# Performance work log

Hardware: AMD Instinct MI355X
Metric: run time of the kernel (lower is better)

## Reference

```python
import jax, jax.numpy as jnp
import numpy as np

EPS = 1e-5

def _ln(x, g, b):
    m = jnp.mean(x, axis=-1, keepdims=True)
    v = jnp.var(x, axis=-1, keepdims=True)
    return (x - m) / jnp.sqrt(v + EPS) * g + b

def setup_inputs() -> dict:
    key = jax.random.key(0)
    ks = jax.random.split(key, 16)
    B, N, CZ, C = 1, 512, 128, 16
    s_cz = 1.0 / np.sqrt(CZ)
    s_c = 1.0 / np.sqrt(C)
    def lin(k, fan_in, shape):
        return jax.random.uniform(k, shape, jnp.float32, -1.0, 1.0) / np.sqrt(fan_in)
    return {
        'x': jax.random.normal(ks[0], (B, N, N, CZ), jnp.float32),
        'Wa1': lin(ks[1], CZ, (CZ, C)), 'ba1': lin(ks[2], CZ, (C,)),
        'Wa2': lin(ks[3], CZ, (CZ, C)), 'ba2': lin(ks[4], CZ, (C,)),
        'Wb1': lin(ks[5], CZ, (CZ, C)), 'bb1': lin(ks[6], CZ, (C,)),
        'Wb2': lin(ks[7], CZ, (CZ, C)), 'bb2': lin(ks[8], CZ, (C,)),
        'ln2_g': jnp.ones((C,), jnp.float32), 'ln2_b': jnp.zeros((C,), jnp.float32),
        'Wg': lin(ks[9], CZ, (CZ, CZ)), 'bg': lin(ks[10], CZ, (CZ,)),
        'Wz': lin(ks[11], C, (C, CZ)), 'bz': lin(ks[12], C, (CZ,)),
    }

def reference(x, Wa1, ba1, Wa2, ba2, Wb1, bb1, Wb2, bb2, ln2_g, ln2_b, Wg, bg, Wz, bz):
    # NOTE: original code computes z=ln1(x) then overwrites z=x, so ln1 is a no-op.
    direction = 'outgoing'
    a = jax.nn.sigmoid((x @ Wa1 + ba1) * (x @ Wa2 + ba2))  # [B,N,N,c]
    b = jax.nn.sigmoid((x @ Wb1 + bb1) * (x @ Wb2 + bb2))  # [B,N,N,c]
    if direction == 'incoming':
        a = jnp.swapaxes(a, 1, 2)
        b = jnp.swapaxes(b, 1, 2)
    g = jax.nn.sigmoid(x @ Wg + bg)  # [B,N,N,c_z]
    # z[b,i,j,c] = sum_k a[b,i,k,c] * b[b,k,j,c]  (per-channel triangle matmul)
    z = jnp.einsum('bikc,bkjc->bijc', a, b)
    return g * (_ln(z, ln2_g, ln2_b) @ Wz + bz)
```

## Files before the change

### kernel.cpp

```cpp
#include <hip/hip_runtime.h>


#define NN 512
#define PP (NN*NN)
#define CZD 128
#define CD 16
#define LN_EPS 1e-5f

typedef unsigned short u16;
typedef __bf16 bf16x8 __attribute__((ext_vector_type(8)));
typedef float  f32x4  __attribute__((ext_vector_type(4)));

#define OFF_A  0u
#define OFF_B  8388608u
#define OFF_Z  16777216u
#define OFF_G  33554432u
#define OFF_WT 100663296u
#define OFF_BC 100712448u

__device__ __forceinline__ float bf2f(u16 u) {
    union { unsigned int i; float f; } v; v.i = ((unsigned int)u) << 16; return v.f;
}
__device__ __forceinline__ u16 f2bf(float f) {
    union { float f; unsigned int i; } v; v.f = f;
    unsigned int r = (v.i + 0x7FFFu + ((v.i >> 16) & 1u)) >> 16;
    return (u16)r;
}
__device__ __forceinline__ float sigmoidf(float x) { return 1.0f / (1.0f + __expf(-x)); }

__global__ void pack_w(const float* __restrict__ Wa1, const float* __restrict__ Wa2,
                       const float* __restrict__ Wb1, const float* __restrict__ Wb2,
                       const float* __restrict__ Wg,
                       const float* __restrict__ ba1, const float* __restrict__ ba2,
                       const float* __restrict__ bb1, const float* __restrict__ bb2,
                       const float* __restrict__ bg,
                       u16* __restrict__ wt, float* __restrict__ bc) {
    int idx = blockIdx.x * 256 + threadIdx.x;
    int n = idx >> 7, k = idx & 127;
    float v;
    if      (n < 16) v = Wa1[k * CD + n];
    else if (n < 32) v = Wa2[k * CD + (n - 16)];
    else if (n < 48) v = Wb1[k * CD + (n - 32)];
    else if (n < 64) v = Wb2[k * CD + (n - 48)];
    else             v = Wg [k * CZD + (n - 64)];
    wt[n * CZD + k] = f2bf(v);
    if (idx < 192) {
        float b;
        if      (idx < 16) b = ba1[idx];
        else if (idx < 32) b = ba2[idx - 16];
        else if (idx < 48) b = bb1[idx - 32];
        else if (idx < 64) b = bb2[idx - 48];
        else               b = bg [idx - 64];
        bc[idx] = b;
    }
}

__global__ __launch_bounds__(256) void proj_kernel(const float* __restrict__ x,
                                                   const u16* __restrict__ wt,
                                                   const float* __restrict__ bc,
                                                   u16* __restrict__ a_ws, u16* __restrict__ b_ws,
                                                   u16* __restrict__ g_ws) {
    __shared__ __align__(16) u16 Xlds[32][136];
    const int t = threadIdx.x;
    const int wave = t >> 6, lane = t & 63;
    const int l16 = lane & 15, quad = lane >> 4;
    const int rt = wave & 1, cg = wave >> 1;
    const long rowBase = (long)blockIdx.x * 32;

#pragma unroll
    for (int i = 0; i < 2; ++i) {
        int chunk = t + 256 * i;
        int r = chunk >> 4, ko = (chunk & 15) << 3;
        const float* xp = x + (rowBase + r) * CZD + ko;
        const float4 v0 = *reinterpret_cast<const float4*>(xp);
        const float4 v1 = *reinterpret_cast<const float4*>(xp + 4);
        u16 tmp[8] = { f2bf(v0.x), f2bf(v0.y), f2bf(v0.z), f2bf(v0.w),
                       f2bf(v1.x), f2bf(v1.y), f2bf(v1.z), f2bf(v1.w) };
        *reinterpret_cast<uint4*>(&Xlds[r][ko]) = *reinterpret_cast<const uint4*>(tmp);
    }
    bf16x8 wb[6][4];
#pragma unroll
    for (int ct = 0; ct < 6; ++ct) {
        int n = cg * 96 + ct * 16 + l16;
#pragma unroll
        for (int ks = 0; ks < 4; ++ks)
            wb[ct][ks] = *reinterpret_cast<const bf16x8*>(wt + n * CZD + ks * 32 + quad * 8);
    }
    __syncthreads();

    f32x4 acc[6];
#pragma unroll
    for (int ct = 0; ct < 6; ++ct) acc[ct] = (f32x4){0.f, 0.f, 0.f, 0.f};
#pragma unroll
    for (int ks = 0; ks < 4; ++ks) {
        bf16x8 af = *reinterpret_cast<const bf16x8*>(&Xlds[rt * 16 + l16][ks * 32 + quad * 8]);
#pragma unroll
        for (int ct = 0; ct < 6; ++ct)
            acc[ct] = __builtin_amdgcn_mfma_f32_16x16x32_bf16(af, wb[ct][ks], acc[ct], 0, 0, 0);
    }

    const int rl = rt * 16 + quad * 4;
    if (cg == 0) {
        const float b0 = bc[l16], b1 = bc[16 + l16], b2 = bc[32 + l16], b3 = bc[48 + l16];
        const float b4 = bc[64 + l16], b5 = bc[80 + l16];
#pragma unroll
        for (int r = 0; r < 4; ++r) {
            long pos = rowBase + rl + r;
            float av = sigmoidf((acc[0][r] + b0) * (acc[1][r] + b1));
            float bv = sigmoidf((acc[2][r] + b2) * (acc[3][r] + b3));
            a_ws[(long)l16 * PP + pos] = f2bf(av);
            b_ws[(long)l16 * PP + pos] = f2bf(bv);
            g_ws[pos * CZD + l16]      = f2bf(sigmoidf(acc[4][r] + b4));
            g_ws[pos * CZD + 16 + l16] = f2bf(sigmoidf(acc[5][r] + b5));
        }
    } else {
        float bb[6];
#pragma unroll
        for (int ct = 0; ct < 6; ++ct) bb[ct] = bc[96 + ct * 16 + l16];
#pragma unroll
        for (int r = 0; r < 4; ++r) {
            long pos = rowBase + rl + r;
#pragma unroll
            for (int ct = 0; ct < 6; ++ct)
                g_ws[pos * CZD + 32 + ct * 16 + l16] = f2bf(sigmoidf(acc[ct][r] + bb[ct]));
        }
    }
}

__global__ __launch_bounds__(256) void tri_kernel(const u16* __restrict__ a_ws,
                                                  const u16* __restrict__ b_ws,
                                                  float* __restrict__ z_ws) {
    __shared__ __align__(16) u16 Alds[64][72];
    __shared__ __align__(16) u16 Btl[64][72];
    const int t = threadIdx.x;
    const int wave = t >> 6, lane = t & 63, l16 = lane & 15, quad = lane >> 4;
    const int c = blockIdx.y;
    const int i0 = (blockIdx.x >> 3) * 64, j0 = (blockIdx.x & 7) * 64;
    const u16* Ap = a_ws + (long)c * PP;
    const u16* Bp = b_ws + (long)c * PP;

    f32x4 acc[4];
#pragma unroll
    for (int ct = 0; ct < 4; ++ct) acc[ct] = (f32x4){0.f, 0.f, 0.f, 0.f};

    for (int k0 = 0; k0 < NN; k0 += 64) {
#pragma unroll
        for (int i = 0; i < 2; ++i) {
            int chunk = t + 256 * i;
            int r = chunk >> 3, ko = (chunk & 7) << 3;
            uint4 v = *reinterpret_cast<const uint4*>(Ap + (long)(i0 + r) * NN + k0 + ko);
            *reinterpret_cast<uint4*>(&Alds[r][ko]) = v;
        }
#pragma unroll
        for (int i = 0; i < 2; ++i) {
            int chunk = t + 256 * i;
            int j = chunk & 63, kg = chunk >> 6;
            u16 tmp[8];
#pragma unroll
            for (int kk = 0; kk < 8; ++kk)
                tmp[kk] = Bp[(long)(k0 + kg * 8 + kk) * NN + j0 + j];
            *reinterpret_cast<uint4*>(&Btl[j][(kg ^ (j & 7)) << 3]) = *reinterpret_cast<uint4*>(tmp);
        }
        __syncthreads();
#pragma unroll
        for (int kk = 0; kk < 64; kk += 32) {
            bf16x8 af = *reinterpret_cast<const bf16x8*>(&Alds[wave * 16 + l16][kk + quad * 8]);
            int kc = (kk >> 3) + quad;
#pragma unroll
            for (int ct = 0; ct < 4; ++ct) {
                int n = ct * 16 + l16;
                bf16x8 bfv = *reinterpret_cast<const bf16x8*>(&Btl[n][(kc ^ (n & 7)) << 3]);
                acc[ct] = __builtin_amdgcn_mfma_f32_16x16x32_bf16(af, bfv, acc[ct], 0, 0, 0);
            }
        }
        __syncthreads();
    }
    float* Zp = z_ws + (long)c * PP;
#pragma unroll
    for (int ct = 0; ct < 4; ++ct)
#pragma unroll
        for (int r = 0; r < 4; ++r)
            Zp[(long)(i0 + wave * 16 + quad * 4 + r) * NN + j0 + ct * 16 + l16] = acc[ct][r];
}

__global__ __launch_bounds__(256) void out_kernel(const float* __restrict__ z_ws,
                                                  const u16* __restrict__ g_ws,
                                                  const float* __restrict__ Wz, const float* __restrict__ bz,
                                                  const float* __restrict__ lng, const float* __restrict__ lnb,
                                                  float* __restrict__ out) {
    __shared__ __align__(16) float zt[16][72];
    __shared__ __align__(16) float nl[64][20];
    __shared__ __align__(16) float wz[16][128];
    __shared__ float bzl[128];
    __shared__ float lg[16], lb[16];
    const int t = threadIdx.x;
    const long pos0 = (long)blockIdx.x * 64;

    {
        int cc = t >> 4, off = (t & 15) << 2;
        const float4 v = *reinterpret_cast<const float4*>(z_ws + (long)cc * PP + pos0 + off);
        *reinterpret_cast<float4*>(&zt[cc][off]) = v;
    }
#pragma unroll
    for (int i = 0; i < 8; ++i) {
        int idx = t + 256 * i;
        wz[idx >> 7][idx & 127] = Wz[idx];
    }
    if (t < 128)      bzl[t] = bz[t];
    else if (t < 144) lg[t - 128] = lng[t - 128];
    else if (t < 160) lb[t - 144] = lnb[t - 144];
    __syncthreads();

    {
        int p = t & 63, cgr = t >> 6;
        float m = 0.f;
#pragma unroll
        for (int c0 = 0; c0 < 16; ++c0) m += zt[c0][p];
        m *= (1.f / 16.f);
        float v = 0.f;
#pragma unroll
        for (int c0 = 0; c0 < 16; ++c0) { float d = zt[c0][p] - m; v += d * d; }
        v *= (1.f / 16.f);
        float s = rsqrtf(v + LN_EPS);
#pragma unroll
        for (int cc = 0; cc < 4; ++cc) {
            int c0 = cgr * 4 + cc;
            nl[p][c0] = (zt[c0][p] - m) * s * lg[c0] + lb[c0];
        }
    }
    __syncthreads();

    const int cz = t & 127, pg = t >> 7;
    float wzr[16];
#pragma unroll
    for (int c0 = 0; c0 < 16; ++c0) wzr[c0] = wz[c0][cz];
    const float bzv = bzl[cz];
#pragma unroll
    for (int pp2 = 0; pp2 < 32; ++pp2) {
        int p = pg * 32 + pp2;
        const float4* np = reinterpret_cast<const float4*>(&nl[p][0]);
        float y = bzv;
#pragma unroll
        for (int c4 = 0; c4 < 4; ++c4) {
            float4 nv = np[c4];
            y += nv.x * wzr[c4 * 4 + 0] + nv.y * wzr[c4 * 4 + 1] +
                 nv.z * wzr[c4 * 4 + 2] + nv.w * wzr[c4 * 4 + 3];
        }
        long o = (pos0 + p) * CZD + cz;
        float gv = bf2f(g_ws[o]);
        out[o] = gv * y;
    }
}

extern "C" void kernel_launch(void* const* d_in, const int* in_sizes, int n_in,
                              void* d_out, int out_size, void* d_ws, size_t ws_size,
                              hipStream_t stream) {
    const float* x   = (const float*)d_in[0];
    const float* Wa1 = (const float*)d_in[1];
    const float* ba1 = (const float*)d_in[2];
    const float* Wa2 = (const float*)d_in[3];
    const float* ba2 = (const float*)d_in[4];
    const float* Wb1 = (const float*)d_in[5];
    const float* bb1 = (const float*)d_in[6];
    const float* Wb2 = (const float*)d_in[7];
    const float* bb2 = (const float*)d_in[8];
    const float* lng = (const float*)d_in[9];
    const float* lnb = (const float*)d_in[10];
    const float* Wg  = (const float*)d_in[11];
    const float* bg  = (const float*)d_in[12];
    const float* Wz  = (const float*)d_in[13];
    const float* bz  = (const float*)d_in[14];
    float* out = (float*)d_out;
    char* ws = (char*)d_ws;
    u16*   a_ws = (u16*)(ws + OFF_A);
    u16*   b_ws = (u16*)(ws + OFF_B);
    float* z_ws = (float*)(ws + OFF_Z);
    u16*   g_ws = (u16*)(ws + OFF_G);
    u16*   wt   = (u16*)(ws + OFF_WT);
    float* bc   = (float*)(ws + OFF_BC);

    hipLaunchKernelGGL(pack_w, dim3(96), dim3(256), 0, stream,
                       Wa1, Wa2, Wb1, Wb2, Wg, ba1, ba2, bb1, bb2, bg, wt, bc);
    hipLaunchKernelGGL(proj_kernel, dim3(8192), dim3(256), 0, stream, x, wt, bc, a_ws, b_ws, g_ws);
    hipLaunchKernelGGL(tri_kernel, dim3(64, 16), dim3(256), 0, stream, a_ws, b_ws, z_ws);
    hipLaunchKernelGGL(out_kernel, dim3(4096), dim3(256), 0, stream, z_ws, g_ws, Wz, bz, lng, lnb, out);
}
```

Measured before the change: 372.3 us.

## Transpose B once, enlarge triangle-matmul tiles, and coalesce projection stores via LDS

The projection kernel now processes 64 rows per block with all 192 output columns per wave. It stages the a, b and g results in shared memory so they go to global memory as coalesced 16-byte stores instead of scattered 2-byte writes. A new transpose kernel writes b in k-contiguous layout, reusing the z workspace as scratch. The triangle matmul uses 128x128 tiles with a 4x4 MFMA grid per wave and register prefetch of the next k-tile, which replaces strided scalar gathers of b and improves data reuse. The cost is an extra kernel launch with a read and write pass over b, plus higher register and LDS use that may lower occupancy.

```diff
diff --git a/kernel.cpp b/kernel.cpp
--- a/kernel.cpp
+++ b/kernel.cpp
@@ -11,12 +11,12 @@
 typedef __bf16 bf16x8 __attribute__((ext_vector_type(8)));
 typedef float  f32x4  __attribute__((ext_vector_type(4)));
 
-#define OFF_A  0u
-#define OFF_B  8388608u
-#define OFF_Z  16777216u
-#define OFF_G  33554432u
-#define OFF_WT 100663296u
-#define OFF_BC 100712448u
+#define OFF_A   0u
+#define OFF_BT  8388608u
+#define OFF_Z   16777216u
+#define OFF_G   33554432u
+#define OFF_WT  100663296u
+#define OFF_BC  100712448u
 
 __device__ __forceinline__ float bf2f(u16 u) {
     union { unsigned int i; float f; } v; v.i = ((unsigned int)u) << 16; return v.f;
@@ -60,127 +60,177 @@
                                                    const float* __restrict__ bc,
                                                    u16* __restrict__ a_ws, u16* __restrict__ b_ws,
                                                    u16* __restrict__ g_ws) {
-    __shared__ __align__(16) u16 Xlds[32][136];
+    __shared__ __align__(16) u16 Xl[64][136];
+    __shared__ __align__(16) u16 at[16][72];
+    __shared__ __align__(16) u16 btl[16][72];
+    __shared__ __align__(16) u16 gt[64][136];
     const int t = threadIdx.x;
-    const int wave = t >> 6, lane = t & 63;
-    const int l16 = lane & 15, quad = lane >> 4;
-    const int rt = wave & 1, cg = wave >> 1;
-    const long rowBase = (long)blockIdx.x * 32;
-
-#pragma unroll
-    for (int i = 0; i < 2; ++i) {
-        int chunk = t + 256 * i;
-        int r = chunk >> 4, ko = (chunk & 15) << 3;
-        const float* xp = x + (rowBase + r) * CZD + ko;
+    const int rt = t >> 6, lane = t & 63, l16 = lane & 15, quad = lane >> 4;
+    const long R0 = (long)blockIdx.x * 64;
+
+#pragma unroll
+    for (int i = 0; i < 4; ++i) {
+        int ch = t + 256 * i;
+        int r = ch >> 4, ko = (ch & 15) << 3;
+        const float* xp = x + (R0 + r) * CZD + ko;
         const float4 v0 = *reinterpret_cast<const float4*>(xp);
         const float4 v1 = *reinterpret_cast<const float4*>(xp + 4);
         u16 tmp[8] = { f2bf(v0.x), f2bf(v0.y), f2bf(v0.z), f2bf(v0.w),
                        f2bf(v1.x), f2bf(v1.y), f2bf(v1.z), f2bf(v1.w) };
-        *reinterpret_cast<uint4*>(&Xlds[r][ko]) = *reinterpret_cast<const uint4*>(tmp);
-    }
-    bf16x8 wb[6][4];
-#pragma unroll
-    for (int ct = 0; ct < 6; ++ct) {
-        int n = cg * 96 + ct * 16 + l16;
-#pragma unroll
-        for (int ks = 0; ks < 4; ++ks)
-            wb[ct][ks] = *reinterpret_cast<const bf16x8*>(wt + n * CZD + ks * 32 + quad * 8);
-    }
-    __syncthreads();
-
-    f32x4 acc[6];
-#pragma unroll
-    for (int ct = 0; ct < 6; ++ct) acc[ct] = (f32x4){0.f, 0.f, 0.f, 0.f};
+        *reinterpret_cast<uint4*>(&Xl[r][ko]) = *reinterpret_cast<const uint4*>(tmp);
+    }
+    const float bA1 = bc[l16], bA2 = bc[16 + l16], bB1 = bc[32 + l16], bB2 = bc[48 + l16];
+    float bG[8];
+#pragma unroll
+    for (int c2 = 0; c2 < 8; ++c2) bG[c2] = bc[64 + c2 * 16 + l16];
+    __syncthreads();
+
+    f32x4 acc[12];
+#pragma unroll
+    for (int ct = 0; ct < 12; ++ct) acc[ct] = (f32x4){0.f, 0.f, 0.f, 0.f};
 #pragma unroll
     for (int ks = 0; ks < 4; ++ks) {
-        bf16x8 af = *reinterpret_cast<const bf16x8*>(&Xlds[rt * 16 + l16][ks * 32 + quad * 8]);
-#pragma unroll
-        for (int ct = 0; ct < 6; ++ct)
-            acc[ct] = __builtin_amdgcn_mfma_f32_16x16x32_bf16(af, wb[ct][ks], acc[ct], 0, 0, 0);
-    }
-
-    const int rl = rt * 16 + quad * 4;
-    if (cg == 0) {
-        const float b0 = bc[l16], b1 = bc[16 + l16], b2 = bc[32 + l16], b3 = bc[48 + l16];
-        const float b4 = bc[64 + l16], b5 = bc[80 + l16];
-#pragma unroll
-        for (int r = 0; r < 4; ++r) {
-            long pos = rowBase + rl + r;
-            float av = sigmoidf((acc[0][r] + b0) * (acc[1][r] + b1));
-            float bv = sigmoidf((acc[2][r] + b2) * (acc[3][r] + b3));
-            a_ws[(long)l16 * PP + pos] = f2bf(av);
-            b_ws[(long)l16 * PP + pos] = f2bf(bv);
-            g_ws[pos * CZD + l16]      = f2bf(sigmoidf(acc[4][r] + b4));
-            g_ws[pos * CZD + 16 + l16] = f2bf(sigmoidf(acc[5][r] + b5));
-        }
+        bf16x8 af = *reinterpret_cast<const bf16x8*>(&Xl[rt * 16 + l16][ks * 32 + quad * 8]);
+#pragma unroll
+        for (int ct = 0; ct < 12; ++ct) {
+            bf16x8 wf = *reinterpret_cast<const bf16x8*>(wt + (ct * 16 + l16) * CZD + ks * 32 + quad * 8);
+            acc[ct] = __builtin_amdgcn_mfma_f32_16x16x32_bf16(af, wf, acc[ct], 0, 0, 0);
+        }
+    }
+
+#pragma unroll
+    for (int r = 0; r < 4; ++r) {
+        int row = rt * 16 + quad * 4 + r;
+        float av = sigmoidf((acc[0][r] + bA1) * (acc[1][r] + bA2));
+        float bv = sigmoidf((acc[2][r] + bB1) * (acc[3][r] + bB2));
+        at[l16][row]  = f2bf(av);
+        btl[l16][row] = f2bf(bv);
+#pragma unroll
+        for (int c2 = 0; c2 < 8; ++c2)
+            gt[row][c2 * 16 + l16] = f2bf(sigmoidf(acc[4 + c2][r] + bG[c2]));
+    }
+    __syncthreads();
+
+    if (t < 128) {
+        int c = t >> 3, ch = t & 7;
+        *reinterpret_cast<uint4*>(a_ws + (long)c * PP + R0 + ch * 8) =
+            *reinterpret_cast<const uint4*>(&at[c][ch * 8]);
     } else {
-        float bb[6];
-#pragma unroll
-        for (int ct = 0; ct < 6; ++ct) bb[ct] = bc[96 + ct * 16 + l16];
-#pragma unroll
-        for (int r = 0; r < 4; ++r) {
-            long pos = rowBase + rl + r;
-#pragma unroll
-            for (int ct = 0; ct < 6; ++ct)
-                g_ws[pos * CZD + 32 + ct * 16 + l16] = f2bf(sigmoidf(acc[ct][r] + bb[ct]));
-        }
+        int c = (t - 128) >> 3, ch = (t - 128) & 7;
+        *reinterpret_cast<uint4*>(b_ws + (long)c * PP + R0 + ch * 8) =
+            *reinterpret_cast<const uint4*>(&btl[c][ch * 8]);
+    }
+#pragma unroll
+    for (int i = 0; i < 4; ++i) {
+        int ch = t + 256 * i;
+        int row = ch >> 4, co = (ch & 15) << 3;
+        *reinterpret_cast<uint4*>(g_ws + (R0 + row) * CZD + co) =
+            *reinterpret_cast<const uint4*>(&gt[row][co]);
+    }
+}
+
+__global__ __launch_bounds__(256) void transpose_b(const u16* __restrict__ b_ws,
+                                                   u16* __restrict__ bt_ws) {
+    __shared__ __align__(16) u16 T[64][72];
+    const int t = threadIdx.x;
+    const int c = blockIdx.y;
+    const int ty = blockIdx.x >> 3, tx = blockIdx.x & 7;
+    const int r0 = ty * 64, c0 = tx * 64;
+    const u16* Bp = b_ws + (long)c * PP;
+    u16* Tp = bt_ws + (long)c * PP;
+#pragma unroll
+    for (int i = 0; i < 2; ++i) {
+        int ch = t + 256 * i;
+        int r = ch >> 3, cc = ch & 7;
+        uint4 v = *reinterpret_cast<const uint4*>(Bp + (long)(r0 + r) * NN + c0 + cc * 8);
+        *reinterpret_cast<uint4*>(&T[r][(cc ^ (r >> 3)) << 3]) = v;
+    }
+    __syncthreads();
+#pragma unroll
+    for (int i = 0; i < 2; ++i) {
+        int ch = t + 256 * i;
+        int j = ch >> 3, s = ch & 7;
+        u16 tmp[8];
+#pragma unroll
+        for (int m = 0; m < 8; ++m) {
+            int row = s * 8 + m;
+            int col = (((j >> 3) ^ s) << 3) + (j & 7);
+            tmp[m] = T[row][col];
+        }
+        *reinterpret_cast<uint4*>(Tp + (long)(c0 + j) * NN + r0 + s * 8) =
+            *reinterpret_cast<const uint4*>(tmp);
     }
 }
 
 __global__ __launch_bounds__(256) void tri_kernel(const u16* __restrict__ a_ws,
-                                                  const u16* __restrict__ b_ws,
+                                                  const u16* __restrict__ bt_ws,
                                                   float* __restrict__ z_ws) {
-    __shared__ __align__(16) u16 Alds[64][72];
-    __shared__ __align__(16) u16 Btl[64][72];
+    __shared__ __align__(16) u16 As[128][72];
+    __shared__ __align__(16) u16 Bs[128][72];
     const int t = threadIdx.x;
-    const int wave = t >> 6, lane = t & 63, l16 = lane & 15, quad = lane >> 4;
+    const int w = t >> 6, lane = t & 63, l16 = lane & 15, quad = lane >> 4;
+    const int wr = w >> 1, wc = w & 1;
     const int c = blockIdx.y;
-    const int i0 = (blockIdx.x >> 3) * 64, j0 = (blockIdx.x & 7) * 64;
+    const int i0 = (blockIdx.x >> 2) * 128, j0 = (blockIdx.x & 3) * 128;
     const u16* Ap = a_ws + (long)c * PP;
-    const u16* Bp = b_ws + (long)c * PP;
-
-    f32x4 acc[4];
-#pragma unroll
-    for (int ct = 0; ct < 4; ++ct) acc[ct] = (f32x4){0.f, 0.f, 0.f, 0.f};
-
-    for (int k0 = 0; k0 < NN; k0 += 64) {
-#pragma unroll
-        for (int i = 0; i < 2; ++i) {
-            int chunk = t + 256 * i;
-            int r = chunk >> 3, ko = (chunk & 7) << 3;
-            uint4 v = *reinterpret_cast<const uint4*>(Ap + (long)(i0 + r) * NN + k0 + ko);
-            *reinterpret_cast<uint4*>(&Alds[r][ko]) = v;
-        }
-#pragma unroll
-        for (int i = 0; i < 2; ++i) {
-            int chunk = t + 256 * i;
-            int j = chunk & 63, kg = chunk >> 6;
-            u16 tmp[8];
-#pragma unroll
-            for (int kk = 0; kk < 8; ++kk)
-                tmp[kk] = Bp[(long)(k0 + kg * 8 + kk) * NN + j0 + j];
-            *reinterpret_cast<uint4*>(&Btl[j][(kg ^ (j & 7)) << 3]) = *reinterpret_cast<uint4*>(tmp);
+    const u16* Bp = bt_ws + (long)c * PP;
+    const int rb = t >> 3, ko0 = (t & 7) << 3;
+
+    f32x4 acc[4][4];
+#pragma unroll
+    for (int i = 0; i < 4; ++i)
+#pragma unroll
+        for (int j = 0; j < 4; ++j) acc[i][j] = (f32x4){0.f, 0.f, 0.f, 0.f};
+
+    uint4 ar[4], br[4];
+#pragma unroll
+    for (int i = 0; i < 4; ++i) {
+        int r = rb + 32 * i;
+        ar[i] = *reinterpret_cast<const uint4*>(Ap + (long)(i0 + r) * NN + ko0);
+        br[i] = *reinterpret_cast<const uint4*>(Bp + (long)(j0 + r) * NN + ko0);
+    }
+    for (int kt = 0; kt < 8; ++kt) {
+#pragma unroll
+        for (int i = 0; i < 4; ++i) {
+            int r = rb + 32 * i;
+            *reinterpret_cast<uint4*>(&As[r][ko0]) = ar[i];
+            *reinterpret_cast<uint4*>(&Bs[r][ko0]) = br[i];
         }
         __syncthreads();
-#pragma unroll
-        for (int kk = 0; kk < 64; kk += 32) {
-            bf16x8 af = *reinterpret_cast<const bf16x8*>(&Alds[wave * 16 + l16][kk + quad * 8]);
-            int kc = (kk >> 3) + quad;
-#pragma unroll
-            for (int ct = 0; ct < 4; ++ct) {
-                int n = ct * 16 + l16;
-                bf16x8 bfv = *reinterpret_cast<const bf16x8*>(&Btl[n][(kc ^ (n & 7)) << 3]);
-                acc[ct] = __builtin_amdgcn_mfma_f32_16x16x32_bf16(af, bfv, acc[ct], 0, 0, 0);
+        if (kt < 7) {
+            int k0 = (kt + 1) * 64;
+#pragma unroll
+            for (int i = 0; i < 4; ++i) {
+                int r = rb + 32 * i;
+                ar[i] = *reinterpret_cast<const uint4*>(Ap + (long)(i0 + r) * NN + k0 + ko0);
+                br[i] = *reinterpret_cast<const uint4*>(Bp + (long)(j0 + r) * NN + k0 + ko0);
             }
         }
+#pragma unroll
+        for (int kk = 0; kk < 2; ++kk) {
+            bf16x8 afr[4], bfr[4];
+#pragma unroll
+            for (int i = 0; i < 4; ++i) {
+                afr[i] = *reinterpret_cast<const bf16x8*>(&As[wr * 64 + i * 16 + l16][kk * 32 + quad * 8]);
+                bfr[i] = *reinterpret_cast<const bf16x8*>(&Bs[wc * 64 + i * 16 + l16][kk * 32 + quad * 8]);
+            }
+#pragma unroll
+            for (int ri = 0; ri < 4; ++ri)
+#pragma unroll
+                for (int ci = 0; ci < 4; ++ci)
+                    acc[ri][ci] = __builtin_amdgcn_mfma_f32_16x16x32_bf16(afr[ri], bfr[ci], acc[ri][ci], 0, 0, 0);
+        }
         __syncthreads();
     }
     float* Zp = z_ws + (long)c * PP;
 #pragma unroll
-    for (int ct = 0; ct < 4; ++ct)
-#pragma unroll
-        for (int r = 0; r < 4; ++r)
-            Zp[(long)(i0 + wave * 16 + quad * 4 + r) * NN + j0 + ct * 16 + l16] = acc[ct][r];
+    for (int ri = 0; ri < 4; ++ri)
+#pragma unroll
+        for (int ci = 0; ci < 4; ++ci)
+#pragma unroll
+            for (int r = 0; r < 4; ++r)
+                Zp[(long)(i0 + wr * 64 + ri * 16 + quad * 4 + r) * NN + j0 + wc * 64 + ci * 16 + l16] =
+                    acc[ri][ci][r];
 }
 
 __global__ __launch_bounds__(256) void out_kernel(const float* __restrict__ z_ws,
@@ -272,16 +322,18 @@
     const float* bz  = (const float*)d_in[14];
     float* out = (float*)d_out;
     char* ws = (char*)d_ws;
-    u16*   a_ws = (u16*)(ws + OFF_A);
-    u16*   b_ws = (u16*)(ws + OFF_B);
-    float* z_ws = (float*)(ws + OFF_Z);
-    u16*   g_ws = (u16*)(ws + OFF_G);
-    u16*   wt   = (u16*)(ws + OFF_WT);
-    float* bc   = (float*)(ws + OFF_BC);
+    u16*   a_ws  = (u16*)(ws + OFF_A);
+    u16*   bt_ws = (u16*)(ws + OFF_BT);
+    u16*   b_ws  = (u16*)(ws + OFF_Z);
+    float* z_ws  = (float*)(ws + OFF_Z);
+    u16*   g_ws  = (u16*)(ws + OFF_G);
+    u16*   wt    = (u16*)(ws + OFF_WT);
+    float* bc    = (float*)(ws + OFF_BC);
 
     hipLaunchKernelGGL(pack_w, dim3(96), dim3(256), 0, stream,
                        Wa1, Wa2, Wb1, Wb2, Wg, ba1, ba2, bb1, bb2, bg, wt, bc);
-    hipLaunchKernelGGL(proj_kernel, dim3(8192), dim3(256), 0, stream, x, wt, bc, a_ws, b_ws, g_ws);
-    hipLaunchKernelGGL(tri_kernel, dim3(64, 16), dim3(256), 0, stream, a_ws, b_ws, z_ws);
+    hipLaunchKernelGGL(proj_kernel, dim3(4096), dim3(256), 0, stream, x, wt, bc, a_ws, b_ws, g_ws);
+    hipLaunchKernelGGL(transpose_b, dim3(64, 16), dim3(256), 0, stream, b_ws, bt_ws);
+    hipLaunchKernelGGL(tri_kernel, dim3(16, 16), dim3(256), 0, stream, a_ws, bt_ws, z_ws);
     hipLaunchKernelGGL(out_kernel, dim3(4096), dim3(256), 0, stream, z_ws, g_ws, Wz, bz, lng, lnb, out);
 }
```

After: 418.2 us. +12.3%, slower.
